# Performance work log

Measured on AMD Instinct MI355X. Metric: run time of the kernel, lower is better.

The kernel has to match this reference:

```python
import jax, jax.numpy as jnp
import numpy as np

N_NODES = 50000


def _gcn_conv(x, src, dst, W, b, n):
    # PyG GCNConv: linear transform, add self-loops, symmetric norm, scatter-sum, bias.
    h = x @ W  # [N, out]
    loop = jnp.arange(n, dtype=src.dtype)
    s = jnp.concatenate([src, loop])
    d = jnp.concatenate([dst, loop])
    deg = jax.ops.segment_sum(jnp.ones_like(d, dtype=h.dtype), d, num_segments=n)
    dinv = jax.lax.rsqrt(jnp.maximum(deg, 1.0))  # deg >= 1 thanks to self-loops
    norm = dinv[s] * dinv[d]  # [E+N]
    msg = h[s] * norm[:, None]
    out = jax.ops.segment_sum(msg, d, num_segments=n)
    return out + b


def setup_inputs() -> dict:
    key = jax.random.key(0)
    ks = jax.random.split(key, 8)
    N, E = N_NODES, 800000
    d_in, d_hid, d_out = 128, 64, 128
    x = jax.random.normal(ks[0], (N, d_in), dtype=jnp.float32)
    edge_index = jax.random.randint(ks[1], (2, E), 0, N, dtype=jnp.int64)
    s = 1.0 / np.sqrt(d_in)
    W1 = jax.random.normal(ks[2], (d_in, d_hid), dtype=jnp.float32) * s
    b1 = jnp.zeros((d_hid,), dtype=jnp.float32)
    Wl = jax.random.normal(ks[3], (d_hid, d_out), dtype=jnp.float32) * (1.0 / np.sqrt(d_hid))
    bl = jnp.zeros((d_out,), dtype=jnp.float32)
    W2 = jax.random.normal(ks[4], (d_hid, d_out), dtype=jnp.float32) * (1.0 / np.sqrt(d_hid))
    b2 = jnp.zeros((d_out,), dtype=jnp.float32)
    return {"x": x, "edge_index": edge_index, "W1": W1, "b1": b1,
            "Wl": Wl, "bl": bl, "W2": W2, "b2": b2}


def reference(x, edge_index, W1, b1, Wl, bl, W2, b2):
    n = x.shape[0]
    src, dst = edge_index[0], edge_index[1]
    h = _gcn_conv(x, src, dst, W1, b1, n)          # conv1 -> [N, 64]
    x1 = h @ Wl + bl                               # residual linear branch [N, 128]
    h = jax.nn.relu(h)
    out = _gcn_conv(h, src, dst, W2, b2, n)        # conv2 -> [N, 128]
    return out + x + x1
```

## Files before the change

### kernel.cpp

```cpp
#include <hip/hip_runtime.h>
#include <hip/hip_fp16.h>

#define DIN 128
#define DH 64
#define DOUT 128
#define STRIDE 64
#define NPART 8

__global__ __launch_bounds__(256) void k_fill(const int* __restrict__ src,
                                              const int* __restrict__ dst,
                                              int* __restrict__ cnt,
                                              unsigned short* __restrict__ csr,
                                              int E, int n) {
  const int part = blockIdx.x & (NPART - 1);
  const int pb = blockIdx.x >> 3;
  const int nblk = gridDim.x >> 3;
  const int lo = (int)((long)part * n / NPART);
  const int hi = (int)((long)(part + 1) * n / NPART);
  for (int e = pb * 256 + threadIdx.x; e < E; e += nblk * 256) {
    int d = dst[e];
    if (d >= lo && d < hi) {
      int slot = atomicAdd(&cnt[d], 1);
      if (slot < STRIDE) csr[(long)d * STRIDE + slot] = (unsigned short)src[e];
    }
  }
}

__global__ __launch_bounds__(256) void k_gemm1(const float* __restrict__ x,
                                               const float* __restrict__ W1,
                                               const int* __restrict__ cnt,
                                               __half* __restrict__ h0p, int n) {
  const int t = threadIdx.x;
  __shared__ float Ws[DIN * DH];
  __shared__ float xs[32][DIN + 4];
  for (int i = t; i < DIN * DH; i += 256) Ws[i] = W1[i];
  const int row0 = blockIdx.x * 32;
  for (int i = t; i < 32 * (DIN / 4); i += 256) {
    int r = i >> 5;
    int k4 = (i & 31) * 4;
    float4 v = make_float4(0.f, 0.f, 0.f, 0.f);
    int row = row0 + r;
    if (row < n) v = *(const float4*)&x[(long)row * DIN + k4];
    *(float4*)&xs[r][k4] = v;
  }
  __syncthreads();
  const int tc = t & 15, tr = t >> 4;
  const int col4 = tc * 4, r0 = tr * 2;
  float acc[2][4];
#pragma unroll
  for (int r = 0; r < 2; r++)
#pragma unroll
    for (int c = 0; c < 4; c++) acc[r][c] = 0.f;
  for (int k4 = 0; k4 < DIN; k4 += 4) {
    float4 xv[2];
#pragma unroll
    for (int r = 0; r < 2; r++) xv[r] = *(const float4*)&xs[r0 + r][k4];
#pragma unroll
    for (int kk = 0; kk < 4; kk++) {
      float4 wv = *(const float4*)&Ws[(k4 + kk) * DH + col4];
#pragma unroll
      for (int r = 0; r < 2; r++) {
        float xval = (&xv[r].x)[kk];
        acc[r][0] = fmaf(xval, wv.x, acc[r][0]);
        acc[r][1] = fmaf(xval, wv.y, acc[r][1]);
        acc[r][2] = fmaf(xval, wv.z, acc[r][2]);
        acc[r][3] = fmaf(xval, wv.w, acc[r][3]);
      }
    }
  }
#pragma unroll
  for (int r = 0; r < 2; r++) {
    int row = row0 + r0 + r;
    if (row < n) {
      float dd = rsqrtf(1.0f + (float)min(cnt[row], STRIDE));
      union { uint2 u; __half2 h[2]; } sv;
      sv.h[0] = __floats2half2_rn(acc[r][0] * dd, acc[r][1] * dd);
      sv.h[1] = __floats2half2_rn(acc[r][2] * dd, acc[r][3] * dd);
      *(uint2*)&h0p[(long)row * DH + col4] = sv.u;
    }
  }
}

__global__ __launch_bounds__(256) void k_gather1(const int* __restrict__ cnt,
                                                 const unsigned short* __restrict__ csr,
                                                 const __half* __restrict__ h0p,
                                                 const float* __restrict__ b1,
                                                 __half* __restrict__ hd, int n) {
  long gid = (long)blockIdx.x * 256 + threadIdx.x;
  int node = (int)(gid >> 3);
  if (node >= n) return;
  int l = (int)(gid & 7);
  const int deg = min(cnt[node], STRIDE);
  const float dd = rsqrtf(1.0f + (float)deg);
  const long base = (long)node * STRIDE;
  float acc[8];
#pragma unroll
  for (int k = 0; k < 8; k++) acc[k] = 0.f;

  auto edge = [&](int s) {
    union { uint4 u; __half2 h[4]; } c;
    c.u = *(const uint4*)&h0p[(long)s * DH + l * 8];
#pragma unroll
    for (int k = 0; k < 4; k++) {
      float2 f = __half22float2(c.h[k]);
      acc[2 * k] += f.x;
      acc[2 * k + 1] += f.y;
    }
  };

  int j = 0;
  for (; j + 4 <= deg; j += 4) {
    ushort4 cs = *(const ushort4*)&csr[base + j];
    edge(cs.x); edge(cs.y); edge(cs.z); edge(cs.w);
  }
  for (; j < deg; j++) edge(csr[base + j]);
  edge(node);

  float4 ba = *(const float4*)&b1[l * 8];
  float4 bb = *(const float4*)&b1[l * 8 + 4];
  float o[8];
  o[0] = acc[0] * dd + ba.x; o[1] = acc[1] * dd + ba.y;
  o[2] = acc[2] * dd + ba.z; o[3] = acc[3] * dd + ba.w;
  o[4] = acc[4] * dd + bb.x; o[5] = acc[5] * dd + bb.y;
  o[6] = acc[6] * dd + bb.z; o[7] = acc[7] * dd + bb.w;
  union { uint4 u; __half2 h[4]; } rv;
#pragma unroll
  for (int k = 0; k < 4; k++)
    rv.h[k] = __floats2half2_rn(o[2 * k] * dd, o[2 * k + 1] * dd);
  *(uint4*)&hd[(long)node * DH + l * 8] = rv.u;
}

__global__ __launch_bounds__(256) void k_gather2C(const int* __restrict__ cnt,
                                                  const unsigned short* __restrict__ csr,
                                                  const __half* __restrict__ hd,
                                                  const float* __restrict__ Wl,
                                                  const float* __restrict__ W2,
                                                  const float* __restrict__ bl,
                                                  const float* __restrict__ b2,
                                                  const float* __restrict__ x,
                                                  float* __restrict__ out, int n) {
  __shared__ float hs[32][DH + 4];
  const int t = threadIdx.x;
  const int row0 = blockIdx.x * 32;

  {
    const int r = t >> 3;
    const int l = t & 7;
    int node = row0 + r;
    float acc[8];
#pragma unroll
    for (int k = 0; k < 8; k++) acc[k] = 0.f;
    float dd = 0.f;
    if (node < n) {
      const int deg = min(cnt[node], STRIDE);
      dd = rsqrtf(1.0f + (float)deg);
      const long base = (long)node * STRIDE;
      auto edge = [&](int s) {
        union { uint4 u; __half2 h[4]; } c;
        c.u = *(const uint4*)&hd[(long)s * DH + l * 8];
#pragma unroll
        for (int k = 0; k < 4; k++) {
          float2 f = __half22float2(c.h[k]);
          acc[2 * k] += fmaxf(f.x, 0.f);
          acc[2 * k + 1] += fmaxf(f.y, 0.f);
        }
      };
      int j = 0;
      for (; j + 4 <= deg; j += 4) {
        ushort4 cs = *(const ushort4*)&csr[base + j];
        edge(cs.x); edge(cs.y); edge(cs.z); edge(cs.w);
      }
      for (; j < deg; j++) edge(csr[base + j]);
      edge(node);
    }
    *(float4*)&hs[r][l * 8] =
        make_float4(acc[0] * dd, acc[1] * dd, acc[2] * dd, acc[3] * dd);
    *(float4*)&hs[r][l * 8 + 4] =
        make_float4(acc[4] * dd, acc[5] * dd, acc[6] * dd, acc[7] * dd);
  }

  const int tc = t & 31, tr = t >> 5;
  const int col4 = tc * 4, r0 = tr * 4;
  float acc[4][4];
#pragma unroll
  for (int r = 0; r < 4; r++)
#pragma unroll
    for (int c = 0; c < 4; c++) acc[r][c] = 0.f;

  __syncthreads();
  for (int k4 = 0; k4 < DH; k4 += 4) {
    float4 hv[4];
#pragma unroll
    for (int r = 0; r < 4; r++) hv[r] = *(const float4*)&hs[r0 + r][k4];
#pragma unroll
    for (int kk = 0; kk < 4; kk++) {
      float4 wv = *(const float4*)&W2[(k4 + kk) * DOUT + col4];
#pragma unroll
      for (int r = 0; r < 4; r++) {
        float hval = (&hv[r].x)[kk];
        acc[r][0] = fmaf(hval, wv.x, acc[r][0]);
        acc[r][1] = fmaf(hval, wv.y, acc[r][1]);
        acc[r][2] = fmaf(hval, wv.z, acc[r][2]);
        acc[r][3] = fmaf(hval, wv.w, acc[r][3]);
      }
    }
  }
  __syncthreads();

  {
    const int r = t >> 3;
    const int l8 = (t & 7) * 8;
    int row = row0 + r;
    float v[8];
#pragma unroll
    for (int k = 0; k < 8; k++) v[k] = 0.f;
    if (row < n) {
      float sc = sqrtf(1.0f + (float)min(cnt[row], STRIDE));
      union { uint4 u; __half2 h[4]; } c;
      c.u = *(const uint4*)&hd[(long)row * DH + l8];
#pragma unroll
      for (int k = 0; k < 4; k++) {
        float2 f = __half22float2(c.h[k]);
        v[2 * k] = f.x * sc;
        v[2 * k + 1] = f.y * sc;
      }
    }
    *(float4*)&hs[r][l8] = make_float4(v[0], v[1], v[2], v[3]);
    *(float4*)&hs[r][l8 + 4] = make_float4(v[4], v[5], v[6], v[7]);
  }
  __syncthreads();
  for (int k4 = 0; k4 < DH; k4 += 4) {
    float4 hv[4];
#pragma unroll
    for (int r = 0; r < 4; r++) hv[r] = *(const float4*)&hs[r0 + r][k4];
#pragma unroll
    for (int kk = 0; kk < 4; kk++) {
      float4 wv = *(const float4*)&Wl[(k4 + kk) * DOUT + col4];
#pragma unroll
      for (int r = 0; r < 4; r++) {
        float hval = (&hv[r].x)[kk];
        acc[r][0] = fmaf(hval, wv.x, acc[r][0]);
        acc[r][1] = fmaf(hval, wv.y, acc[r][1]);
        acc[r][2] = fmaf(hval, wv.z, acc[r][2]);
        acc[r][3] = fmaf(hval, wv.w, acc[r][3]);
      }
    }
  }

  float4 blv = *(const float4*)&bl[col4];
  float4 b2v = *(const float4*)&b2[col4];
#pragma unroll
  for (int r = 0; r < 4; r++) {
    int row = row0 + r0 + r;
    if (row < n) {
      float4 xv = *(const float4*)&x[(long)row * DOUT + col4];
      float4 o;
      o.x = xv.x + acc[r][0] + blv.x + b2v.x;
      o.y = xv.y + acc[r][1] + blv.y + b2v.y;
      o.z = xv.z + acc[r][2] + blv.z + b2v.z;
      o.w = xv.w + acc[r][3] + blv.w + b2v.w;
      *(float4*)&out[(long)row * DOUT + col4] = o;
    }
  }
}

extern "C" void kernel_launch(void* const* d_in, const int* in_sizes, int n_in,
                              void* d_out, int out_size, void* d_ws, size_t ws_size,
                              hipStream_t stream) {
  const float* x = (const float*)d_in[0];
  const int* edge_index = (const int*)d_in[1];
  const float* W1 = (const float*)d_in[2];
  const float* b1 = (const float*)d_in[3];
  const float* Wl = (const float*)d_in[4];
  const float* bl = (const float*)d_in[5];
  const float* W2 = (const float*)d_in[6];
  const float* b2 = (const float*)d_in[7];
  float* out = (float*)d_out;

  const int n = in_sizes[0] / DIN;
  const int E = in_sizes[1] / 2;
  const int* src = edge_index;
  const int* dst = edge_index + E;

  char* p = (char*)d_ws;
  auto alloc = [&](size_t bytes) { char* r = p; p += (bytes + 255) & ~(size_t)255; return r; };
  int* cnt = (int*)alloc((size_t)n * 4);
  unsigned short* csr = (unsigned short*)alloc((size_t)n * STRIDE * 2);
  __half* h0p = (__half*)alloc((size_t)n * DH * 2);
  __half* hd = (__half*)alloc((size_t)n * DH * 2);

  const int B = 256;
  hipMemsetAsync(cnt, 0, (size_t)n * sizeof(int), stream);
  k_fill<<<NPART * 256, B, 0, stream>>>(src, dst, cnt, csr, E, n);
  k_gemm1<<<(n + 31) / 32, B, 0, stream>>>(x, W1, cnt, h0p, n);
  k_gather1<<<(int)(((long)n * 8 + B - 1) / B), B, 0, stream>>>(cnt, csr, h0p, b1, hd, n);
  k_gather2C<<<(n + 31) / 32, B, 0, stream>>>(cnt, csr, hd, Wl, W2, bl, b2, x, out, n);
}
```

Baseline: 205.4 us.

## Partition CSR by source range and aggregate per-partition partials for locality

Adds a path that buckets edges by source-node quarter, so each gather kernel reads a bounded slice of the feature table (better L2 locality). Each partition writes fp16 partial sums, and a reduce or epilogue kernel combines them with the self-loop term. Degree normalization is precomputed once into a dinv array inside the first GEMM. This adds extra launches and partial-buffer traffic (4x N x 64 halfs written and read per layer), plus an extra fp16 rounding of the partials. The old path is kept as a fallback when the workspace is too small.

Result: slower. 224.5 us (+9.3%).

```diff
diff --git a/kernel.cpp b/kernel.cpp
--- a/kernel.cpp
+++ b/kernel.cpp
@@ -4,19 +4,322 @@
 #define DIN 128
 #define DH 64
 #define DOUT 128
+#define NP 4
+#define SUB 24
 #define STRIDE 64
-#define NPART 8
+typedef unsigned int u32x4 __attribute__((ext_vector_type(4)));
+
+
+__global__ __launch_bounds__(256) void k_fill4(const int* __restrict__ src,
+                                               const int* __restrict__ dst,
+                                               int* __restrict__ cnt4,
+                                               unsigned short* __restrict__ csr4,
+                                               int E, int n) {
+  const int part = blockIdx.x & (NP - 1);
+  const int dh = (blockIdx.x >> 2) & 1;
+  const int pb = blockIdx.x >> 3;
+  const int nblk = gridDim.x >> 3;
+  const int slo = (int)((long)part * n / NP);
+  const int shi = (int)((long)(part + 1) * n / NP);
+  const int dlo = (int)((long)dh * n / 2);
+  const int dhi = (int)((long)(dh + 1) * n / 2);
+  for (int e = pb * 256 + threadIdx.x; e < E; e += nblk * 256) {
+    int s = src[e];
+    if (s >= slo && s < shi) {
+      int d = dst[e];
+      if (d >= dlo && d < dhi) {
+        long cell = (long)part * n + d;
+        int slot = atomicAdd(&cnt4[cell], 1);
+        if (slot < SUB) csr4[cell * SUB + slot] = (unsigned short)s;
+      }
+    }
+  }
+}
+
+__global__ __launch_bounds__(256) void k_gemm1n(const float* __restrict__ x,
+                                                const float* __restrict__ W1,
+                                                const int* __restrict__ cnt4,
+                                                __half* __restrict__ h0p,
+                                                float* __restrict__ dinv, int n) {
+  const int t = threadIdx.x;
+  __shared__ float Ws[DIN * DH];
+  __shared__ float xs[32][DIN + 4];
+  __shared__ float dds[32];
+  const int row0 = blockIdx.x * 32;
+  if (t < 32) {
+    int row = row0 + t;
+    float dd = 0.f;
+    if (row < n) {
+      int deg = 0;
+#pragma unroll
+      for (int p = 0; p < NP; p++) deg += min(cnt4[(long)p * n + row], SUB);
+      dd = rsqrtf(1.0f + (float)deg);
+      dinv[row] = dd;
+    }
+    dds[t] = dd;
+  }
+  for (int i = t; i < DIN * DH; i += 256) Ws[i] = W1[i];
+  for (int i = t; i < 32 * (DIN / 4); i += 256) {
+    int r = i >> 5;
+    int k4 = (i & 31) * 4;
+    float4 v = make_float4(0.f, 0.f, 0.f, 0.f);
+    int row = row0 + r;
+    if (row < n) v = *(const float4*)&x[(long)row * DIN + k4];
+    *(float4*)&xs[r][k4] = v;
+  }
+  __syncthreads();
+  const int tc = t & 15, tr = t >> 4;
+  const int col4 = tc * 4, r0 = tr * 2;
+  float acc[2][4];
+#pragma unroll
+  for (int r = 0; r < 2; r++)
+#pragma unroll
+    for (int c = 0; c < 4; c++) acc[r][c] = 0.f;
+  for (int k4 = 0; k4 < DIN; k4 += 4) {
+    float4 xv[2];
+#pragma unroll
+    for (int r = 0; r < 2; r++) xv[r] = *(const float4*)&xs[r0 + r][k4];
+#pragma unroll
+    for (int kk = 0; kk < 4; kk++) {
+      float4 wv = *(const float4*)&Ws[(k4 + kk) * DH + col4];
+#pragma unroll
+      for (int r = 0; r < 2; r++) {
+        float xval = (&xv[r].x)[kk];
+        acc[r][0] = fmaf(xval, wv.x, acc[r][0]);
+        acc[r][1] = fmaf(xval, wv.y, acc[r][1]);
+        acc[r][2] = fmaf(xval, wv.z, acc[r][2]);
+        acc[r][3] = fmaf(xval, wv.w, acc[r][3]);
+      }
+    }
+  }
+#pragma unroll
+  for (int r = 0; r < 2; r++) {
+    int row = row0 + r0 + r;
+    if (row < n) {
+      float dd = dds[r0 + r];
+      union { uint2 u; __half2 h[2]; } sv;
+      sv.h[0] = __floats2half2_rn(acc[r][0] * dd, acc[r][1] * dd);
+      sv.h[1] = __floats2half2_rn(acc[r][2] * dd, acc[r][3] * dd);
+      *(uint2*)&h0p[(long)row * DH + col4] = sv.u;
+    }
+  }
+}
+
+template <bool RELU>
+__global__ __launch_bounds__(256) void k_part(const int* __restrict__ cnt4,
+                                              const unsigned short* __restrict__ csr4,
+                                              const __half* __restrict__ src16,
+                                              __half* __restrict__ pa, int n) {
+  const int part = blockIdx.x & (NP - 1);
+  const int chunk = blockIdx.x >> 2;
+  const int t = threadIdx.x;
+  const int r = t >> 3, l = t & 7;
+  const int d = chunk * 32 + r;
+  if (d >= n) return;
+  const long cell = (long)part * n + d;
+  const int degp = min(cnt4[cell], SUB);
+  const long base = cell * SUB;
+  float acc[8];
+#pragma unroll
+  for (int k = 0; k < 8; k++) acc[k] = 0.f;
+  for (int j = 0; j < degp; j++) {
+    int s = csr4[base + j];
+    union { uint4 u; __half2 h[4]; } c;
+    c.u = *(const uint4*)&src16[(long)s * DH + l * 8];
+#pragma unroll
+    for (int k = 0; k < 4; k++) {
+      float2 f = __half22float2(c.h[k]);
+      if (RELU) { f.x = fmaxf(f.x, 0.f); f.y = fmaxf(f.y, 0.f); }
+      acc[2 * k] += f.x;
+      acc[2 * k + 1] += f.y;
+    }
+  }
+  union { u32x4 u; __half2 h[4]; } pv;
+#pragma unroll
+  for (int k = 0; k < 4; k++) pv.h[k] = __floats2half2_rn(acc[2 * k], acc[2 * k + 1]);
+  __builtin_nontemporal_store(pv.u, (u32x4*)&pa[cell * DH + l * 8]);
+}
+
+__global__ __launch_bounds__(256) void k_red1(const __half* __restrict__ pa,
+                                              const __half* __restrict__ h0p,
+                                              const float* __restrict__ dinv,
+                                              const float* __restrict__ b1,
+                                              __half* __restrict__ hd, int n) {
+  long gid = (long)blockIdx.x * 256 + threadIdx.x;
+  int node = (int)(gid >> 3);
+  if (node >= n) return;
+  int l = (int)(gid & 7);
+  float acc[8];
+#pragma unroll
+  for (int k = 0; k < 8; k++) acc[k] = 0.f;
+#pragma unroll
+  for (int p = 0; p <= NP; p++) {
+    union { uint4 u; __half2 h[4]; } c;
+    const __half* srcp = (p < NP) ? &pa[((long)p * n + node) * DH + l * 8]
+                                  : &h0p[(long)node * DH + l * 8];
+    c.u = *(const uint4*)srcp;
+#pragma unroll
+    for (int k = 0; k < 4; k++) {
+      float2 f = __half22float2(c.h[k]);
+      acc[2 * k] += f.x;
+      acc[2 * k + 1] += f.y;
+    }
+  }
+  const float dd = dinv[node];
+  float4 ba = *(const float4*)&b1[l * 8];
+  float4 bb = *(const float4*)&b1[l * 8 + 4];
+  float o[8];
+  o[0] = acc[0] * dd + ba.x; o[1] = acc[1] * dd + ba.y;
+  o[2] = acc[2] * dd + ba.z; o[3] = acc[3] * dd + ba.w;
+  o[4] = acc[4] * dd + bb.x; o[5] = acc[5] * dd + bb.y;
+  o[6] = acc[6] * dd + bb.z; o[7] = acc[7] * dd + bb.w;
+  union { uint4 u; __half2 h[4]; } rv;
+#pragma unroll
+  for (int k = 0; k < 4; k++)
+    rv.h[k] = __floats2half2_rn(o[2 * k] * dd, o[2 * k + 1] * dd);
+  *(uint4*)&hd[(long)node * DH + l * 8] = rv.u;
+}
+
+__global__ __launch_bounds__(256) void k_epi(const __half* __restrict__ pa,
+                                             const __half* __restrict__ hd,
+                                             const float* __restrict__ dinv,
+                                             const float* __restrict__ Wl,
+                                             const float* __restrict__ W2,
+                                             const float* __restrict__ bl,
+                                             const float* __restrict__ b2,
+                                             const float* __restrict__ x,
+                                             float* __restrict__ out, int n) {
+  __shared__ float hs[32][DH + 4];
+  const int t = threadIdx.x;
+  const int row0 = blockIdx.x * 32;
+
+  {
+    const int r = t >> 3;
+    const int l = t & 7;
+    int node = row0 + r;
+    float acc[8];
+#pragma unroll
+    for (int k = 0; k < 8; k++) acc[k] = 0.f;
+    float dd = 0.f;
+    if (node < n) {
+      dd = dinv[node];
+#pragma unroll
+      for (int p = 0; p <= NP; p++) {
+        union { uint4 u; __half2 h[4]; } c;
+        const __half* srcp = (p < NP) ? &pa[((long)p * n + node) * DH + l * 8]
+                                      : &hd[(long)node * DH + l * 8];
+        c.u = *(const uint4*)srcp;
+#pragma unroll
+        for (int k = 0; k < 4; k++) {
+          float2 f = __half22float2(c.h[k]);
+          if (p == NP) { f.x = fmaxf(f.x, 0.f); f.y = fmaxf(f.y, 0.f); }
+          acc[2 * k] += f.x;
+          acc[2 * k + 1] += f.y;
+        }
+      }
+    }
+    *(float4*)&hs[r][l * 8] =
+        make_float4(acc[0] * dd, acc[1] * dd, acc[2] * dd, acc[3] * dd);
+    *(float4*)&hs[r][l * 8 + 4] =
+        make_float4(acc[4] * dd, acc[5] * dd, acc[6] * dd, acc[7] * dd);
+  }
+
+  const int tc = t & 31, tr = t >> 5;
+  const int col4 = tc * 4, r0 = tr * 4;
+  float acc[4][4];
+#pragma unroll
+  for (int r = 0; r < 4; r++)
+#pragma unroll
+    for (int c = 0; c < 4; c++) acc[r][c] = 0.f;
+
+  __syncthreads();
+  for (int k4 = 0; k4 < DH; k4 += 4) {
+    float4 hv[4];
+#pragma unroll
+    for (int r = 0; r < 4; r++) hv[r] = *(const float4*)&hs[r0 + r][k4];
+#pragma unroll
+    for (int kk = 0; kk < 4; kk++) {
+      float4 wv = *(const float4*)&W2[(k4 + kk) * DOUT + col4];
+#pragma unroll
+      for (int r = 0; r < 4; r++) {
+        float hval = (&hv[r].x)[kk];
+        acc[r][0] = fmaf(hval, wv.x, acc[r][0]);
+        acc[r][1] = fmaf(hval, wv.y, acc[r][1]);
+        acc[r][2] = fmaf(hval, wv.z, acc[r][2]);
+        acc[r][3] = fmaf(hval, wv.w, acc[r][3]);
+      }
+    }
+  }
+  __syncthreads();
+
+  {
+    const int r = t >> 3;
+    const int l8 = (t & 7) * 8;
+    int row = row0 + r;
+    float v[8];
+#pragma unroll
+    for (int k = 0; k < 8; k++) v[k] = 0.f;
+    if (row < n) {
+      float sc = 1.0f / dinv[row];
+      union { uint4 u; __half2 h[4]; } c;
+      c.u = *(const uint4*)&hd[(long)row * DH + l8];
+#pragma unroll
+      for (int k = 0; k < 4; k++) {
+        float2 f = __half22float2(c.h[k]);
+        v[2 * k] = f.x * sc;
+        v[2 * k + 1] = f.y * sc;
+      }
+    }
+    *(float4*)&hs[r][l8] = make_float4(v[0], v[1], v[2], v[3]);
+    *(float4*)&hs[r][l8 + 4] = make_float4(v[4], v[5], v[6], v[7]);
+  }
+  __syncthreads();
+  for (int k4 = 0; k4 < DH; k4 += 4) {
+    float4 hv[4];
+#pragma unroll
+    for (int r = 0; r < 4; r++) hv[r] = *(const float4*)&hs[r0 + r][k4];
+#pragma unroll
+    for (int kk = 0; kk < 4; kk++) {
+      float4 wv = *(const float4*)&Wl[(k4 + kk) * DOUT + col4];
+#pragma unroll
+      for (int r = 0; r < 4; r++) {
+        float hval = (&hv[r].x)[kk];
+        acc[r][0] = fmaf(hval, wv.x, acc[r][0]);
+        acc[r][1] = fmaf(hval, wv.y, acc[r][1]);
+        acc[r][2] = fmaf(hval, wv.z, acc[r][2]);
+        acc[r][3] = fmaf(hval, wv.w, acc[r][3]);
+      }
+    }
+  }
+
+  float4 blv = *(const float4*)&bl[col4];
+  float4 b2v = *(const float4*)&b2[col4];
+#pragma unroll
+  for (int r = 0; r < 4; r++) {
+    int row = row0 + r0 + r;
+    if (row < n) {
+      float4 xv = *(const float4*)&x[(long)row * DOUT + col4];
+      float4 o;
+      o.x = xv.x + acc[r][0] + blv.x + b2v.x;
+      o.y = xv.y + acc[r][1] + blv.y + b2v.y;
+      o.z = xv.z + acc[r][2] + blv.z + b2v.z;
+      o.w = xv.w + acc[r][3] + blv.w + b2v.w;
+      *(float4*)&out[(long)row * DOUT + col4] = o;
+    }
+  }
+}
+
 
 __global__ __launch_bounds__(256) void k_fill(const int* __restrict__ src,
                                               const int* __restrict__ dst,
                                               int* __restrict__ cnt,
                                               unsigned short* __restrict__ csr,
                                               int E, int n) {
-  const int part = blockIdx.x & (NPART - 1);
+  const int part = blockIdx.x & 7;
   const int pb = blockIdx.x >> 3;
   const int nblk = gridDim.x >> 3;
-  const int lo = (int)((long)part * n / NPART);
-  const int hi = (int)((long)(part + 1) * n / NPART);
+  const int lo = (int)((long)part * n / 8);
+  const int hi = (int)((long)(part + 1) * n / 8);
   for (int e = pb * 256 + threadIdx.x; e < E; e += nblk * 256) {
     int d = dst[e];
     if (d >= lo && d < hi) {
@@ -26,10 +329,10 @@
   }
 }
 
-__global__ __launch_bounds__(256) void k_gemm1(const float* __restrict__ x,
-                                               const float* __restrict__ W1,
-                                               const int* __restrict__ cnt,
-                                               __half* __restrict__ h0p, int n) {
+__global__ __launch_bounds__(256) void k_gemm1f(const float* __restrict__ x,
+                                                const float* __restrict__ W1,
+                                                const int* __restrict__ cnt,
+                                                __half* __restrict__ h0p, int n) {
   const int t = threadIdx.x;
   __shared__ float Ws[DIN * DH];
   __shared__ float xs[32][DIN + 4];
@@ -96,7 +399,6 @@
   float acc[8];
 #pragma unroll
   for (int k = 0; k < 8; k++) acc[k] = 0.f;
-
   auto edge = [&](int s) {
     union { uint4 u; __half2 h[4]; } c;
     c.u = *(const uint4*)&h0p[(long)s * DH + l * 8];
@@ -107,7 +409,6 @@
       acc[2 * k + 1] += f.y;
     }
   };
-
   int j = 0;
   for (; j + 4 <= deg; j += 4) {
     ushort4 cs = *(const ushort4*)&csr[base + j];
@@ -115,7 +416,6 @@
   }
   for (; j < deg; j++) edge(csr[base + j]);
   edge(node);
-
   float4 ba = *(const float4*)&b1[l * 8];
   float4 bb = *(const float4*)&b1[l * 8 + 4];
   float o[8];
@@ -142,7 +442,6 @@
   __shared__ float hs[32][DH + 4];
   const int t = threadIdx.x;
   const int row0 = blockIdx.x * 32;
-
   {
     const int r = t >> 3;
     const int l = t & 7;
@@ -178,7 +477,6 @@
     *(float4*)&hs[r][l * 8 + 4] =
         make_float4(acc[4] * dd, acc[5] * dd, acc[6] * dd, acc[7] * dd);
   }
-
   const int tc = t & 31, tr = t >> 5;
   const int col4 = tc * 4, r0 = tr * 4;
   float acc[4][4];
@@ -186,7 +484,6 @@
   for (int r = 0; r < 4; r++)
 #pragma unroll
     for (int c = 0; c < 4; c++) acc[r][c] = 0.f;
-
   __syncthreads();
   for (int k4 = 0; k4 < DH; k4 += 4) {
     float4 hv[4];
@@ -206,7 +503,6 @@
     }
   }
   __syncthreads();
-
   {
     const int r = t >> 3;
     const int l8 = (t & 7) * 8;
@@ -246,7 +542,6 @@
       }
     }
   }
-
   float4 blv = *(const float4*)&bl[col4];
   float4 b2v = *(const float4*)&b2[col4];
 #pragma unroll
@@ -263,6 +558,7 @@
     }
   }
 }
+
 
 extern "C" void kernel_launch(void* const* d_in, const int* in_sizes, int n_in,
                               void* d_out, int out_size, void* d_ws, size_t ws_size,
@@ -281,18 +577,41 @@
   const int E = in_sizes[1] / 2;
   const int* src = edge_index;
   const int* dst = edge_index + E;
+  const int B = 256;
+  const int blocks32 = (n + 31) / 32;
 
   char* p = (char*)d_ws;
   auto alloc = [&](size_t bytes) { char* r = p; p += (bytes + 255) & ~(size_t)255; return r; };
-  int* cnt = (int*)alloc((size_t)n * 4);
-  unsigned short* csr = (unsigned short*)alloc((size_t)n * STRIDE * 2);
-  __half* h0p = (__half*)alloc((size_t)n * DH * 2);
-  __half* hd = (__half*)alloc((size_t)n * DH * 2);
-
-  const int B = 256;
-  hipMemsetAsync(cnt, 0, (size_t)n * sizeof(int), stream);
-  k_fill<<<NPART * 256, B, 0, stream>>>(src, dst, cnt, csr, E, n);
-  k_gemm1<<<(n + 31) / 32, B, 0, stream>>>(x, W1, cnt, h0p, n);
-  k_gather1<<<(int)(((long)n * 8 + B - 1) / B), B, 0, stream>>>(cnt, csr, h0p, b1, hd, n);
-  k_gather2C<<<(n + 31) / 32, B, 0, stream>>>(cnt, csr, hd, Wl, W2, bl, b2, x, out, n);
-}
+
+  const size_t need_new = ((size_t)NP * n * 4 + 256) + ((size_t)NP * n * SUB * 2 + 256) +
+                          ((size_t)n * DH * 2 + 256) * 2 + ((size_t)n * 4 + 256) +
+                          ((size_t)NP * n * DH * 2 + 256);
+
+  if (ws_size >= need_new) {
+    int* cnt4 = (int*)alloc((size_t)NP * n * 4);
+    unsigned short* csr4 = (unsigned short*)alloc((size_t)NP * n * SUB * 2);
+    __half* h0p = (__half*)alloc((size_t)n * DH * 2);
+    __half* hd = (__half*)alloc((size_t)n * DH * 2);
+    float* dinv = (float*)alloc((size_t)n * 4);
+    __half* pa = (__half*)alloc((size_t)NP * n * DH * 2);
+
+    hipMemsetAsync(cnt4, 0, (size_t)NP * n * 4, stream);
+    k_fill4<<<2048, B, 0, stream>>>(src, dst, cnt4, csr4, E, n);
+    k_gemm1n<<<blocks32, B, 0, stream>>>(x, W1, cnt4, h0p, dinv, n);
+    k_part<false><<<NP * blocks32, B, 0, stream>>>(cnt4, csr4, h0p, pa, n);
+    k_red1<<<(int)(((long)n * 8 + B - 1) / B), B, 0, stream>>>(pa, h0p, dinv, b1, hd, n);
+    k_part<true><<<NP * blocks32, B, 0, stream>>>(cnt4, csr4, hd, pa, n);
+    k_epi<<<blocks32, B, 0, stream>>>(pa, hd, dinv, Wl, W2, bl, b2, x, out, n);
+  } else {
+    int* cnt = (int*)alloc((size_t)n * 4);
+    unsigned short* csr = (unsigned short*)alloc((size_t)n * STRIDE * 2);
+    __half* h0p = (__half*)alloc((size_t)n * DH * 2);
+    __half* hd = (__half*)alloc((size_t)n * DH * 2);
+
+    hipMemsetAsync(cnt, 0, (size_t)n * sizeof(int), stream);
+    k_fill<<<8 * 256, B, 0, stream>>>(src, dst, cnt, csr, E, n);
+    k_gemm1f<<<blocks32, B, 0, stream>>>(x, W1, cnt, h0p, n);
+    k_gather1<<<(int)(((long)n * 8 + B - 1) / B), B, 0, stream>>>(cnt, csr, h0p, b1, hd, n);
+    k_gather2C<<<blocks32, B, 0, stream>>>(cnt, csr, hd, Wl, W2, bl, b2, x, out, n);
+  }
+}
```

## Use one wavefront per node for gathers and split epilogue GEMM

Applied to the files above, without the earlier changes.

Both neighbour-aggregation kernels now assign a full 64-lane wavefront to each node: eight edges are processed in parallel, each by eight lanes, and the partial sums are combined with xor shuffles. The old design had eight lanes walk a node's edges one after another, which serialised the dependent loads. The second gather is split out of the fused GEMM kernel and writes an fp32 intermediate that a new epilogue kernel reads back. This adds an extra launch and a 50000x64 fp32 round trip through memory, and leaves lanes idle when a node has few edges (average degree is about 16).

After: 230.3 us. 1.12x slower.

```diff
diff --git a/kernel.cpp b/kernel.cpp
--- a/kernel.cpp
+++ b/kernel.cpp
@@ -6,6 +6,7 @@
 #define DOUT 128
 #define STRIDE 64
 #define NPART 8
+
 
 __global__ __launch_bounds__(256) void k_fill(const int* __restrict__ src,
                                               const int* __restrict__ dst,
@@ -81,102 +82,143 @@
   }
 }
 
-__global__ __launch_bounds__(256) void k_gather1(const int* __restrict__ cnt,
-                                                 const unsigned short* __restrict__ csr,
-                                                 const __half* __restrict__ h0p,
-                                                 const float* __restrict__ b1,
-                                                 __half* __restrict__ hd, int n) {
-  long gid = (long)blockIdx.x * 256 + threadIdx.x;
-  int node = (int)(gid >> 3);
+__global__ __launch_bounds__(256) void k_gather1w(const int* __restrict__ cnt,
+                                                  const unsigned short* __restrict__ csr,
+                                                  const __half* __restrict__ h0p,
+                                                  const float* __restrict__ b1,
+                                                  __half* __restrict__ hd, int n) {
+  const int t = threadIdx.x;
+  const int lane = t & 63;
+  const int e = lane >> 3;
+  const int c = lane & 7;
+  const int node = blockIdx.x * 4 + (t >> 6);
   if (node >= n) return;
-  int l = (int)(gid & 7);
   const int deg = min(cnt[node], STRIDE);
   const float dd = rsqrtf(1.0f + (float)deg);
   const long base = (long)node * STRIDE;
+
   float acc[8];
 #pragma unroll
   for (int k = 0; k < 8; k++) acc[k] = 0.f;
 
-  auto edge = [&](int s) {
-    union { uint4 u; __half2 h[4]; } c;
-    c.u = *(const uint4*)&h0p[(long)s * DH + l * 8];
+  for (int j = 0; j < deg; j += 8) {
+    if (j + e < deg) {
+      int s = csr[base + j + e];
+      union { uint4 u; __half2 h[4]; } cc;
+      cc.u = *(const uint4*)&h0p[(long)s * DH + c * 8];
+#pragma unroll
+      for (int k = 0; k < 4; k++) {
+        float2 f = __half22float2(cc.h[k]);
+        acc[2 * k] += f.x;
+        acc[2 * k + 1] += f.y;
+      }
+    }
+  }
+#pragma unroll
+  for (int k = 0; k < 8; k++) acc[k] += __shfl_xor(acc[k], 8, 64);
+#pragma unroll
+  for (int k = 0; k < 8; k++) acc[k] += __shfl_xor(acc[k], 16, 64);
+#pragma unroll
+  for (int k = 0; k < 8; k++) acc[k] += __shfl_xor(acc[k], 32, 64);
+
+  if (e == 0) {
+    union { uint4 u; __half2 h[4]; } cs;
+    cs.u = *(const uint4*)&h0p[(long)node * DH + c * 8];
 #pragma unroll
     for (int k = 0; k < 4; k++) {
-      float2 f = __half22float2(c.h[k]);
+      float2 f = __half22float2(cs.h[k]);
       acc[2 * k] += f.x;
       acc[2 * k + 1] += f.y;
     }
-  };
-
-  int j = 0;
-  for (; j + 4 <= deg; j += 4) {
-    ushort4 cs = *(const ushort4*)&csr[base + j];
-    edge(cs.x); edge(cs.y); edge(cs.z); edge(cs.w);
-  }
-  for (; j < deg; j++) edge(csr[base + j]);
-  edge(node);
-
-  float4 ba = *(const float4*)&b1[l * 8];
-  float4 bb = *(const float4*)&b1[l * 8 + 4];
-  float o[8];
-  o[0] = acc[0] * dd + ba.x; o[1] = acc[1] * dd + ba.y;
-  o[2] = acc[2] * dd + ba.z; o[3] = acc[3] * dd + ba.w;
-  o[4] = acc[4] * dd + bb.x; o[5] = acc[5] * dd + bb.y;
-  o[6] = acc[6] * dd + bb.z; o[7] = acc[7] * dd + bb.w;
-  union { uint4 u; __half2 h[4]; } rv;
-#pragma unroll
-  for (int k = 0; k < 4; k++)
-    rv.h[k] = __floats2half2_rn(o[2 * k] * dd, o[2 * k + 1] * dd);
-  *(uint4*)&hd[(long)node * DH + l * 8] = rv.u;
-}
-
-__global__ __launch_bounds__(256) void k_gather2C(const int* __restrict__ cnt,
+    float4 ba = *(const float4*)&b1[c * 8];
+    float4 bb = *(const float4*)&b1[c * 8 + 4];
+    float o[8];
+    o[0] = acc[0] * dd + ba.x; o[1] = acc[1] * dd + ba.y;
+    o[2] = acc[2] * dd + ba.z; o[3] = acc[3] * dd + ba.w;
+    o[4] = acc[4] * dd + bb.x; o[5] = acc[5] * dd + bb.y;
+    o[6] = acc[6] * dd + bb.z; o[7] = acc[7] * dd + bb.w;
+    union { uint4 u; __half2 h[4]; } rv;
+#pragma unroll
+    for (int k = 0; k < 4; k++)
+      rv.h[k] = __floats2half2_rn(o[2 * k] * dd, o[2 * k + 1] * dd);
+    *(uint4*)&hd[(long)node * DH + c * 8] = rv.u;
+  }
+}
+
+__global__ __launch_bounds__(256) void k_gather2w(const int* __restrict__ cnt,
                                                   const unsigned short* __restrict__ csr,
                                                   const __half* __restrict__ hd,
-                                                  const float* __restrict__ Wl,
-                                                  const float* __restrict__ W2,
-                                                  const float* __restrict__ bl,
-                                                  const float* __restrict__ b2,
-                                                  const float* __restrict__ x,
-                                                  float* __restrict__ out, int n) {
+                                                  float* __restrict__ z32, int n) {
+  const int t = threadIdx.x;
+  const int lane = t & 63;
+  const int e = lane >> 3;
+  const int c = lane & 7;
+  const int node = blockIdx.x * 4 + (t >> 6);
+  if (node >= n) return;
+  const int deg = min(cnt[node], STRIDE);
+  const float dd = rsqrtf(1.0f + (float)deg);
+  const long base = (long)node * STRIDE;
+
+  float acc[8];
+#pragma unroll
+  for (int k = 0; k < 8; k++) acc[k] = 0.f;
+
+  for (int j = 0; j < deg; j += 8) {
+    if (j + e < deg) {
+      int s = csr[base + j + e];
+      union { uint4 u; __half2 h[4]; } cc;
+      cc.u = *(const uint4*)&hd[(long)s * DH + c * 8];
+#pragma unroll
+      for (int k = 0; k < 4; k++) {
+        float2 f = __half22float2(cc.h[k]);
+        acc[2 * k] += fmaxf(f.x, 0.f);
+        acc[2 * k + 1] += fmaxf(f.y, 0.f);
+      }
+    }
+  }
+#pragma unroll
+  for (int k = 0; k < 8; k++) acc[k] += __shfl_xor(acc[k], 8, 64);
+#pragma unroll
+  for (int k = 0; k < 8; k++) acc[k] += __shfl_xor(acc[k], 16, 64);
+#pragma unroll
+  for (int k = 0; k < 8; k++) acc[k] += __shfl_xor(acc[k], 32, 64);
+
+  if (e == 0) {
+    union { uint4 u; __half2 h[4]; } cs;
+    cs.u = *(const uint4*)&hd[(long)node * DH + c * 8];
+#pragma unroll
+    for (int k = 0; k < 4; k++) {
+      float2 f = __half22float2(cs.h[k]);
+      acc[2 * k] += fmaxf(f.x, 0.f);
+      acc[2 * k + 1] += fmaxf(f.y, 0.f);
+    }
+    *(float4*)&z32[(long)node * DH + c * 8] =
+        make_float4(acc[0] * dd, acc[1] * dd, acc[2] * dd, acc[3] * dd);
+    *(float4*)&z32[(long)node * DH + c * 8 + 4] =
+        make_float4(acc[4] * dd, acc[5] * dd, acc[6] * dd, acc[7] * dd);
+  }
+}
+
+__global__ __launch_bounds__(256) void k_epi(const float* __restrict__ z32,
+                                             const __half* __restrict__ hd,
+                                             const int* __restrict__ cnt,
+                                             const float* __restrict__ Wl,
+                                             const float* __restrict__ W2,
+                                             const float* __restrict__ bl,
+                                             const float* __restrict__ b2,
+                                             const float* __restrict__ x,
+                                             float* __restrict__ out, int n) {
   __shared__ float hs[32][DH + 4];
   const int t = threadIdx.x;
   const int row0 = blockIdx.x * 32;
 
-  {
-    const int r = t >> 3;
-    const int l = t & 7;
-    int node = row0 + r;
-    float acc[8];
-#pragma unroll
-    for (int k = 0; k < 8; k++) acc[k] = 0.f;
-    float dd = 0.f;
-    if (node < n) {
-      const int deg = min(cnt[node], STRIDE);
-      dd = rsqrtf(1.0f + (float)deg);
-      const long base = (long)node * STRIDE;
-      auto edge = [&](int s) {
-        union { uint4 u; __half2 h[4]; } c;
-        c.u = *(const uint4*)&hd[(long)s * DH + l * 8];
-#pragma unroll
-        for (int k = 0; k < 4; k++) {
-          float2 f = __half22float2(c.h[k]);
-          acc[2 * k] += fmaxf(f.x, 0.f);
-          acc[2 * k + 1] += fmaxf(f.y, 0.f);
-        }
-      };
-      int j = 0;
-      for (; j + 4 <= deg; j += 4) {
-        ushort4 cs = *(const ushort4*)&csr[base + j];
-        edge(cs.x); edge(cs.y); edge(cs.z); edge(cs.w);
-      }
-      for (; j < deg; j++) edge(csr[base + j]);
-      edge(node);
-    }
-    *(float4*)&hs[r][l * 8] =
-        make_float4(acc[0] * dd, acc[1] * dd, acc[2] * dd, acc[3] * dd);
-    *(float4*)&hs[r][l * 8 + 4] =
-        make_float4(acc[4] * dd, acc[5] * dd, acc[6] * dd, acc[7] * dd);
+  for (int i = t; i < 32 * (DH / 4); i += 256) {
+    int r = i >> 4;
+    int k4 = (i & 15) * 4;
+    float4 v = make_float4(0.f, 0.f, 0.f, 0.f);
+    int row = row0 + r;
+    if (row < n) v = *(const float4*)&z32[(long)row * DH + k4];
+    *(float4*)&hs[r][k4] = v;
   }
 
   const int tc = t & 31, tr = t >> 5;
@@ -288,11 +330,15 @@
   unsigned short* csr = (unsigned short*)alloc((size_t)n * STRIDE * 2);
   __half* h0p = (__half*)alloc((size_t)n * DH * 2);
   __half* hd = (__half*)alloc((size_t)n * DH * 2);
+  float* z32 = (float*)alloc((size_t)n * DH * 4);
 
   const int B = 256;
+  const int blocks32 = (n + 31) / 32;
+  const int blocks4 = (n + 3) / 4;
   hipMemsetAsync(cnt, 0, (size_t)n * sizeof(int), stream);
   k_fill<<<NPART * 256, B, 0, stream>>>(src, dst, cnt, csr, E, n);
-  k_gemm1<<<(n + 31) / 32, B, 0, stream>>>(x, W1, cnt, h0p, n);
-  k_gather1<<<(int)(((long)n * 8 + B - 1) / B), B, 0, stream>>>(cnt, csr, h0p, b1, hd, n);
-  k_gather2C<<<(n + 31) / 32, B, 0, stream>>>(cnt, csr, hd, Wl, W2, bl, b2, x, out, n);
-}
+  k_gemm1<<<blocks32, B, 0, stream>>>(x, W1, cnt, h0p, n);
+  k_gather1w<<<blocks4, B, 0, stream>>>(cnt, csr, h0p, b1, hd, n);
+  k_gather2w<<<blocks4, B, 0, stream>>>(cnt, csr, hd, z32, n);
+  k_epi<<<blocks32, B, 0, stream>>>(z32, hd, cnt, Wl, W2, bl, b2, x, out, n);
+}
```

## Use fp16 MFMA for first GEMM and reduce fill partitions to four

Applied to the files above, without the earlier changes.

Replaces the scalar fp32 FMA GEMM for x@W1 with fp16 MFMA 16x16x32 instructions, staging x and a transposed W1 in shared memory as fp16 and precomputing the degree normalisation per row. This targets the compute cost of the first linear transform. The fill kernel's destination partitioning also drops from 8 to 4, so each block scans the edge list fewer times at the cost of more atomic contention per partition. The fp16 input rounding loses some precision, and the output stores become scalar half writes instead of vectorised ones.

Result: faster. 197.0 us (-4.1%).

```diff
diff --git a/kernel.cpp b/kernel.cpp
--- a/kernel.cpp
+++ b/kernel.cpp
@@ -5,7 +5,11 @@
 #define DH 64
 #define DOUT 128
 #define STRIDE 64
-#define NPART 8
+#define NPART 4
+
+
+typedef _Float16 f16x8 __attribute__((ext_vector_type(8)));
+typedef float f32x4 __attribute__((ext_vector_type(4)));
 
 __global__ __launch_bounds__(256) void k_fill(const int* __restrict__ src,
                                               const int* __restrict__ dst,
@@ -13,8 +17,8 @@
                                               unsigned short* __restrict__ csr,
                                               int E, int n) {
   const int part = blockIdx.x & (NPART - 1);
-  const int pb = blockIdx.x >> 3;
-  const int nblk = gridDim.x >> 3;
+  const int pb = blockIdx.x >> 2;
+  const int nblk = gridDim.x >> 2;
   const int lo = (int)((long)part * n / NPART);
   const int hi = (int)((long)(part + 1) * n / NPART);
   for (int e = pb * 256 + threadIdx.x; e < E; e += nblk * 256) {
@@ -26,57 +30,54 @@
   }
 }
 
-__global__ __launch_bounds__(256) void k_gemm1(const float* __restrict__ x,
-                                               const float* __restrict__ W1,
-                                               const int* __restrict__ cnt,
-                                               __half* __restrict__ h0p, int n) {
+__global__ __launch_bounds__(256) void k_gemm1m(const float* __restrict__ x,
+                                                const float* __restrict__ W1,
+                                                const int* __restrict__ cnt,
+                                                __half* __restrict__ h0p, int n) {
+  __shared__ _Float16 As[32][DIN + 8];
+  __shared__ _Float16 Bt[DH][DIN + 8];
+  __shared__ float dds[32];
   const int t = threadIdx.x;
-  __shared__ float Ws[DIN * DH];
-  __shared__ float xs[32][DIN + 4];
-  for (int i = t; i < DIN * DH; i += 256) Ws[i] = W1[i];
   const int row0 = blockIdx.x * 32;
+  if (t < 32) {
+    int row = row0 + t;
+    dds[t] = (row < n) ? rsqrtf(1.0f + (float)min(cnt[row], STRIDE)) : 0.f;
+  }
+  for (int i = t; i < DIN * DH; i += 256) {
+    int k = i >> 6, c = i & 63;
+    Bt[c][k] = (_Float16)W1[i];
+  }
   for (int i = t; i < 32 * (DIN / 4); i += 256) {
-    int r = i >> 5;
-    int k4 = (i & 31) * 4;
+    int r = i >> 5, k4 = (i & 31) * 4;
     float4 v = make_float4(0.f, 0.f, 0.f, 0.f);
     int row = row0 + r;
     if (row < n) v = *(const float4*)&x[(long)row * DIN + k4];
-    *(float4*)&xs[r][k4] = v;
+    As[r][k4 + 0] = (_Float16)v.x; As[r][k4 + 1] = (_Float16)v.y;
+    As[r][k4 + 2] = (_Float16)v.z; As[r][k4 + 3] = (_Float16)v.w;
   }
   __syncthreads();
-  const int tc = t & 15, tr = t >> 4;
-  const int col4 = tc * 4, r0 = tr * 2;
-  float acc[2][4];
-#pragma unroll
-  for (int r = 0; r < 2; r++)
-#pragma unroll
-    for (int c = 0; c < 4; c++) acc[r][c] = 0.f;
-  for (int k4 = 0; k4 < DIN; k4 += 4) {
-    float4 xv[2];
-#pragma unroll
-    for (int r = 0; r < 2; r++) xv[r] = *(const float4*)&xs[r0 + r][k4];
-#pragma unroll
-    for (int kk = 0; kk < 4; kk++) {
-      float4 wv = *(const float4*)&Ws[(k4 + kk) * DH + col4];
-#pragma unroll
-      for (int r = 0; r < 2; r++) {
-        float xval = (&xv[r].x)[kk];
-        acc[r][0] = fmaf(xval, wv.x, acc[r][0]);
-        acc[r][1] = fmaf(xval, wv.y, acc[r][1]);
-        acc[r][2] = fmaf(xval, wv.z, acc[r][2]);
-        acc[r][3] = fmaf(xval, wv.w, acc[r][3]);
-      }
-    }
-  }
-#pragma unroll
-  for (int r = 0; r < 2; r++) {
-    int row = row0 + r0 + r;
+
+  const int w = t >> 6, l = t & 63;
+  const int rg = w & 1;
+  const int cg0 = (w >> 1) * 2;
+  const int ia = l & 15, kg = l >> 4;
+  f32x4 acc0 = {0.f, 0.f, 0.f, 0.f}, acc1 = {0.f, 0.f, 0.f, 0.f};
+#pragma unroll
+  for (int kb = 0; kb < DIN; kb += 32) {
+    f16x8 a  = *(const f16x8*)&As[rg * 16 + ia][kb + kg * 8];
+    f16x8 b0 = *(const f16x8*)&Bt[cg0 * 16 + ia][kb + kg * 8];
+    f16x8 b1 = *(const f16x8*)&Bt[(cg0 + 1) * 16 + ia][kb + kg * 8];
+    acc0 = __builtin_amdgcn_mfma_f32_16x16x32_f16(a, b0, acc0, 0, 0, 0);
+    acc1 = __builtin_amdgcn_mfma_f32_16x16x32_f16(a, b1, acc1, 0, 0, 0);
+  }
+#pragma unroll
+  for (int reg = 0; reg < 4; reg++) {
+    int rr = rg * 16 + kg * 4 + reg;
+    int row = row0 + rr;
     if (row < n) {
-      float dd = rsqrtf(1.0f + (float)min(cnt[row], STRIDE));
-      union { uint2 u; __half2 h[2]; } sv;
-      sv.h[0] = __floats2half2_rn(acc[r][0] * dd, acc[r][1] * dd);
-      sv.h[1] = __floats2half2_rn(acc[r][2] * dd, acc[r][3] * dd);
-      *(uint2*)&h0p[(long)row * DH + col4] = sv.u;
+      float dd = dds[rr];
+      h0p[(long)row * DH + cg0 * 16 + ia] = (__half)(acc0[reg] * dd);
+      h0p[(long)row * DH + (cg0 + 1) * 16 + ia] = (__half)(acc1[reg] * dd);
     }
   }
 }
@@ -290,9 +291,10 @@
   __half* hd = (__half*)alloc((size_t)n * DH * 2);
 
   const int B = 256;
+  const int blocks32 = (n + 31) / 32;
   hipMemsetAsync(cnt, 0, (size_t)n * sizeof(int), stream);
   k_fill<<<NPART * 256, B, 0, stream>>>(src, dst, cnt, csr, E, n);
-  k_gemm1<<<(n + 31) / 32, B, 0, stream>>>(x, W1, cnt, h0p, n);
+  k_gemm1m<<<blocks32, B, 0, stream>>>(x, W1, cnt, h0p, n);
   k_gather1<<<(int)(((long)n * 8 + B - 1) / B), B, 0, stream>>>(cnt, csr, h0p, b1, hd, n);
-  k_gather2C<<<(n + 31) / 32, B, 0, stream>>>(cnt, csr, hd, Wl, W2, bl, b2, x, out, n);
-}
+  k_gather2C<<<blocks32, B, 0, stream>>>(cnt, csr, hd, Wl, W2, bl, b2, x, out, n);
+}
```
